# Kernel tuning notes

Hardware: AMD Instinct MI355X
Metric: run time of the kernel (lower is better)

Reference implementation:

```python
import jax, jax.numpy as jnp
import numpy as np

SCALE = 256.0  # emulates SharedFxpShift = 8 fixed-point shift


def requant(x):
    # RequantFxpToScaledInt8: shift down by SharedFxpShift and clamp to int8 range
    return jnp.clip(x / SCALE, -128.0, 127.0)


def prelu(x, a):
    return jnp.where(x >= 0, x, a * x)


def _linearize(c):
    # injective encoding of 3D int coords (coords in [-8, 2040) after +8 shift)
    c = c.astype(jnp.int64) + 8
    B = 2048
    return (c[:, 0] * B + c[:, 1]) * B + c[:, 2]


def sparse_conv(coords, feats, W, stride):
    # 3x3x3 submanifold sparse conv: for each kernel offset, hash-lookup the
    # neighbor via sorted linearized coords + searchsorted, gather, matmul.
    # coords [N,3] int32, feats [N,Cin], W [27,Cin,Cout]
    lin = _linearize(coords)
    perm = jnp.argsort(lin)
    slin = lin[perm]
    N = coords.shape[0]
    out = jnp.zeros((N, W.shape[-1]), feats.dtype)
    k = 0
    for dx in (-1, 0, 1):
        for dy in (-1, 0, 1):
            for dz in (-1, 0, 1):
                off = jnp.array([dx, dy, dz], jnp.int32) * stride
                q = _linearize(coords + off[None, :])
                pos = jnp.clip(jnp.searchsorted(slin, q), 0, N - 1)
                hit = slin[pos] == q
                nb = perm[pos]
                f = jnp.where(hit[:, None], feats[nb], 0.0)
                out = out + f @ W[k]
                k += 1
    return out


def setup_inputs() -> dict:
    N, M, C = 200000, 400000, 64
    rng = np.random.default_rng(0)
    # unique parent coords: multiples of 2 in 512^3 grid
    lin = rng.choice(2 ** 24, size=N, replace=False).astype(np.int64)
    px = (lin // (256 * 256)) % 256
    py = (lin // 256) % 256
    pz = lin % 256
    rec_C = (np.stack([px, py, pz], 1) * 2).astype(np.int32)  # [N,3], stride 2
    # exactly M occupied children out of N*8, sorted (row-major mask order)
    child_idx = np.sort(rng.choice(N * 8, size=M, replace=False)).astype(np.int32)
    parent = child_idx // 8
    bit = child_idx % 8
    off = np.stack([(bit >> 2) & 1, (bit >> 1) & 1, bit & 1], 1).astype(np.int32)
    child_C = rec_C[parent] + off  # [M,3], stride 1, unique
    bins1_bits = np.zeros((N, 8), np.int32)
    bins1_bits[parent, bit] = 1
    bins0_bits = rng.integers(0, 2, size=(M, 8)).astype(np.int32)

    key = jax.random.key(0)
    ks = jax.random.split(key, 20)

    def w(k, shape, fan_in):
        return jax.random.normal(k, shape, jnp.float32) / np.sqrt(fan_in)

    inp = {
        "rec_F": jax.random.normal(ks[0], (N, C), jnp.float32) * SCALE,
        "dec_W": w(ks[1], (C + 8, C), C + 8),
        "dec_b": w(ks[2], (C,), 1) * 0.1,
        "dec_a": jnp.full((C,), 0.25, jnp.float32),
        "res_W1": w(ks[3], (27, C, C), 27 * C),
        "res_b1": w(ks[4], (C,), 1) * 0.1,
        "res_a1": jnp.full((C,), 0.25, jnp.float32),
        "res_W2": w(ks[5], (27, C, C), 27 * C),
        "res_b2": w(ks[6], (C,), 1) * 0.1,
        "p0_Wc": w(ks[7], (27, C, C), 27 * C),
        "p0_bc": w(ks[8], (C,), 1) * 0.1,
        "p0_ac": jnp.full((C,), 0.25, jnp.float32),
        "p0_Wl": w(ks[9], (C, C * 8), C),
        "p1_Wc": w(ks[10], (27, C, C), 27 * C),
        "p1_bc": w(ks[11], (C,), 1) * 0.1,
        "p1_ac": jnp.full((C,), 0.25, jnp.float32),
        "p1_Wl": w(ks[12], (C, 255), C),
        "rec_C": jnp.asarray(rec_C),
        "bins1_bits": jnp.asarray(bins1_bits),
        "child_idx": jnp.asarray(child_idx),
        "child_C": jnp.asarray(child_C),
        "bins0_bits": jnp.asarray(bins0_bits),
    }
    return inp


def reference(rec_F, dec_W, dec_b, dec_a, res_W1, res_b1, res_a1, res_W2, res_b2,
              p0_Wc, p0_bc, p0_ac, p0_Wl, p1_Wc, p1_bc, p1_ac, p1_Wl,
              rec_C, bins1_bits, child_idx, child_C, bins0_bits):
    C = dec_W.shape[1]
    # embed (empty Sequential for pred_steps=2): bins1.F << SharedFxpShift
    embed_f = bins1_bits.astype(jnp.float32) * SCALE  # [N,8]
    x = jnp.concatenate([rec_F, embed_f], 1)  # [N, C+8]
    # dec: Requant -> LinearPReLU(C+8 -> C, out32) -> ResBlock(C)
    h = requant(x)
    h = prelu(h @ dec_W + dec_b, dec_a)  # [N,C]
    r = requant(h)
    r = prelu(sparse_conv(rec_C, r, res_W1, 2) + res_b1, res_a1)
    r = requant(r)
    r = sparse_conv(rec_C, r, res_W2, 2) + res_b2
    rec_out = h + r  # [N,C]
    # pred[0]: Requant -> SparseConvPReLU(out8) -> Linear(C -> 8C, out32)
    p = requant(rec_out)
    p = requant(prelu(sparse_conv(rec_C, p, p0_Wc, 2) + p0_bc, p0_ac))
    p = p @ p0_Wl  # [N, 8C]
    # boolean-mask gather of occupied children: reshape [N,8,C] then mask ->
    # equals flat row gather with precomputed sorted child indices
    p = p.reshape(-1, C)[child_idx]  # [M,C]
    # pred[1] (last): Requant -> SparseConvPReLU(out8) -> Linear(C -> 255, out32)
    p = requant(p)
    p = requant(prelu(sparse_conv(child_C, p, p1_Wc, 1) + p1_bc, p1_ac))
    pred_out = p @ p1_Wl  # [M,255]
    # cur_oct = (cur_bins[0].F << bin2oct_kernel).sum(1) - 1
    k = jnp.arange(8, dtype=jnp.int32)
    cur_oct = ((bins0_bits << k).sum(1) - 1).astype(jnp.int16)  # [M]
    return rec_out, pred_out, cur_oct
```

## Files before the change

### kernel.cpp

```cpp
#include <hip/hip_runtime.h>
#include <stdint.h>


typedef short bf16x8 __attribute__((ext_vector_type(8)));
typedef float f32x4 __attribute__((ext_vector_type(4)));

#define EMPTY_KEY 0xFFFFFFFFu

__device__ __forceinline__ float rq(float x) {
  x *= (1.0f / 256.0f);
  return fminf(fmaxf(x, -128.0f), 127.0f);
}

__device__ __forceinline__ short f2b(float f) {
  union { float f; uint32_t u; } v; v.f = f;
  uint32_t u = v.u;
  uint32_t r = (u + 0x7FFFu + ((u >> 16) & 1u)) >> 16;
  return (short)r;
}

__device__ __forceinline__ uint32_t hkey(int x, int y, int z) {
  return ((uint32_t)(x + 8) << 20) | ((uint32_t)(y + 8) << 10) | (uint32_t)(z + 8);
}
__device__ __forceinline__ uint32_t hfun(uint32_t key, uint32_t mask) {
  return (key * 2654435761u) & mask;
}


__global__ void k_fill_u32(uint32_t* p, int n, uint32_t v) {
  int i = blockIdx.x * 256 + threadIdx.x;
  if (i < n) p[i] = v;
}

__global__ void k_hash_insert(const int* __restrict__ coords, int n,
                              uint32_t* __restrict__ keys, int* __restrict__ vals,
                              uint32_t mask) {
  int i = blockIdx.x * 256 + threadIdx.x;
  if (i >= n) return;
  uint32_t key = hkey(coords[i * 3], coords[i * 3 + 1], coords[i * 3 + 2]);
  uint32_t s = hfun(key, mask);
  while (true) {
    uint32_t old = atomicCAS(&keys[s], EMPTY_KEY, key);
    if (old == EMPTY_KEY) { vals[s] = i; return; }
    s = (s + 1) & mask;
  }
}

__global__ void k_build_nbr(const int* __restrict__ coords, int n, int stride,
                            const uint32_t* __restrict__ keys,
                            const int* __restrict__ vals, uint32_t mask,
                            int* __restrict__ nbr) {
  int t = blockIdx.x * 256 + threadIdx.x;
  if (t >= n * 27) return;
  int i = t / 27, k = t % 27;
  int dx = k / 9 - 1, dy = (k / 3) % 3 - 1, dz = k % 3 - 1;
  int x = coords[i * 3] + dx * stride;
  int y = coords[i * 3 + 1] + dy * stride;
  int z = coords[i * 3 + 2] + dz * stride;
  uint32_t key = hkey(x, y, z);
  uint32_t s = hfun(key, mask);
  int res = -1;
  while (true) {
    uint32_t kk = keys[s];
    if (kk == key) { res = vals[s]; break; }
    if (kk == EMPTY_KEY) break;
    s = (s + 1) & mask;
  }
  nbr[(size_t)i * 28 + k] = res;
}

__global__ void k_pack_bits(const int* __restrict__ bins1, int N,
                            int* __restrict__ bitsPacked) {
  int p = blockIdx.x * 256 + threadIdx.x;
  if (p >= N) return;
  int b = 0;
#pragma unroll
  for (int e = 0; e < 8; e++) b |= (bins1[(size_t)p * 8 + e] & 1) << e;
  bitsPacked[p] = b;
}

__global__ void k_parent_start(const int* __restrict__ child_idx, int M,
                               int* __restrict__ ps) {
  int m = blockIdx.x * 256 + threadIdx.x;
  if (m >= M) return;
  int p = child_idx[m] >> 3;
  if (m == 0 || (child_idx[m - 1] >> 3) != p) ps[p] = m;
}

__global__ void k_build_nbr_child(const int* __restrict__ child_C,
                                  const int* __restrict__ child_idx, int M,
                                  const uint32_t* __restrict__ rkeys,
                                  const int* __restrict__ rvals, uint32_t rmask,
                                  const int* __restrict__ bitsPacked,
                                  const int* __restrict__ parentStart,
                                  int* __restrict__ nbr) {
  int t = blockIdx.x * 256 + threadIdx.x;
  if (t >= M * 27) return;
  int m = t / 27, k = t % 27;
  int dx = k / 9 - 1, dy = (k / 3) % 3 - 1, dz = k % 3 - 1;
  int cx = child_C[(size_t)m * 3], cy = child_C[(size_t)m * 3 + 1],
      cz = child_C[(size_t)m * 3 + 2];
  int tx = cx + dx, ty = cy + dy, tz = cz + dz;
  int qx = tx >> 1, qy = ty >> 1, qz = tz >> 1;
  int r;
  if (qx == (cx >> 1) && qy == (cy >> 1) && qz == (cz >> 1)) {
    r = child_idx[m] >> 3;
  } else {
    uint32_t key = hkey(qx * 2, qy * 2, qz * 2);
    uint32_t s = hfun(key, rmask);
    r = -1;
    while (true) {
      uint32_t kk = rkeys[s];
      if (kk == key) { r = rvals[s]; break; }
      if (kk == EMPTY_KEY) break;
      s = (s + 1) & rmask;
    }
  }
  int res = -1;
  if (r >= 0) {
    int bits = bitsPacked[r];
    int bit = ((tx & 1) << 2) | ((ty & 1) << 1) | (tz & 1);
    if ((bits >> bit) & 1)
      res = parentStart[r] + __popc(bits & ((1 << bit) - 1));
  }
  nbr[(size_t)m * 28 + k] = res;
}

__global__ void k_pack_conv(const float* __restrict__ W, short* __restrict__ dst) {
  int gid = blockIdx.x * 256 + threadIdx.x;
  if (gid >= 27 * 2 * 4 * 64) return;
  int lane = gid & 63;
  int c = (gid >> 6) & 3;
  int t = (gid >> 8) & 1;
  int k = gid >> 9;
  int n = c * 16 + (lane & 15);
  int g = lane >> 4;
  bf16x8 v;
#pragma unroll
  for (int e = 0; e < 8; e++) {
    int kk = t * 32 + g * 8 + e;
    v[e] = f2b(W[(k * 64 + kk) * 64 + n]);
  }
  *(bf16x8*)(dst + gid * 8) = v;
}

__global__ void k_pack_dense(const float* __restrict__ W, short* __restrict__ dst,
                             int K, int Ncols, int KT, int CT) {
  int gid = blockIdx.x * 256 + threadIdx.x;
  if (gid >= KT * CT * 64) return;
  int lane = gid & 63;
  int c = (gid >> 6) % CT;
  int t = gid / (64 * CT);
  int n = c * 16 + (lane & 15);
  int g = lane >> 4;
  bf16x8 v;
#pragma unroll
  for (int e = 0; e < 8; e++) {
    int kk = t * 32 + g * 8 + e;
    float val = (kk < K && n < Ncols) ? W[kk * Ncols + n] : 0.0f;
    v[e] = f2b(val);
  }
  *(bf16x8*)(dst + gid * 8) = v;
}

__global__ void __launch_bounds__(256)
k_bucket(const int* __restrict__ child_idx, int M,
         int* __restrict__ lists, int* __restrict__ cnt) {
  __shared__ int lcnt[8];
  __shared__ int lbase[8];
  int tid = threadIdx.x;
  if (tid < 8) lcnt[tid] = 0;
  __syncthreads();
  int m = blockIdx.x * 256 + tid;
  int b = 0, lp = 0;
  if (m < M) {
    b = child_idx[m] & 7;
    lp = atomicAdd(&lcnt[b], 1);
  }
  __syncthreads();
  if (tid < 8) lbase[tid] = atomicAdd(&cnt[tid], lcnt[tid]);
  __syncthreads();
  if (m < M) lists[(size_t)b * M + lbase[b] + lp] = m;
}


__global__ void __launch_bounds__(256)
k_dec(const float* __restrict__ recF, const int* __restrict__ bits,
      const short* __restrict__ wp, const float* __restrict__ bias,
      const float* __restrict__ alpha, float* __restrict__ h32,
      short* __restrict__ hq) {
  int tid = threadIdx.x, wid = tid >> 6, lane = tid & 63;
  int rowbase = blockIdx.x * 64 + wid * 16;
  int lrow = rowbase + (lane & 15);
  int g = lane >> 4;
  f32x4 acc[4] = {};
#pragma unroll
  for (int t = 0; t < 3; t++) {
    bf16x8 a = {0, 0, 0, 0, 0, 0, 0, 0};
    if (t < 2) {
      const float* src = recF + (size_t)lrow * 64 + t * 32 + g * 8;
#pragma unroll
      for (int e = 0; e < 8; e++) a[e] = f2b(rq(src[e]));
    } else if (g == 0) {
      const int* bp = bits + (size_t)lrow * 8;
#pragma unroll
      for (int e = 0; e < 8; e++) a[e] = f2b((float)bp[e]);
    }
#pragma unroll
    for (int c = 0; c < 4; c++) {
      bf16x8 b = *(const bf16x8*)(wp + ((t * 4 + c) * 64 + lane) * 8);
      acc[c] = __builtin_amdgcn_mfma_f32_16x16x32_bf16(a, b, acc[c], 0, 0, 0);
    }
  }
#pragma unroll
  for (int c = 0; c < 4; c++) {
    int col = c * 16 + (lane & 15);
    float bi = bias[col], al = alpha[col];
#pragma unroll
    for (int r = 0; r < 4; r++) {
      int row = rowbase + g * 4 + r;
      float v = acc[c][r] + bi;
      v = v >= 0.0f ? v : al * v;
      h32[(size_t)row * 64 + col] = v;
      hq[(size_t)row * 64 + col] = f2b(rq(v));
    }
  }
}

template <int MODE>
__global__ void __launch_bounds__(256)
k_conv(const short* __restrict__ fin, const int* __restrict__ nbr,
       const short* __restrict__ wp, const float* __restrict__ bias,
       const float* __restrict__ alpha, const float* __restrict__ resid,
       float* __restrict__ out32, short* __restrict__ outq) {
  int tid = threadIdx.x, wid = tid >> 6, lane = tid & 63;
  int rowbase = blockIdx.x * 64 + wid * 16;
  int lrow = rowbase + (lane & 15);
  int g = lane >> 4;

  int4 nv[7];
#pragma unroll
  for (int j = 0; j < 7; j++)
    nv[j] = *(const int4*)(nbr + (size_t)lrow * 28 + j * 4);
  int nbk[28];
#pragma unroll
  for (int j = 0; j < 7; j++) {
    nbk[j * 4 + 0] = nv[j].x;
    nbk[j * 4 + 1] = nv[j].y;
    nbk[j * 4 + 2] = nv[j].z;
    nbk[j * 4 + 3] = nv[j].w;
  }

  f32x4 acc[4] = {};
#pragma unroll
  for (int k = 0; k < 27; k++) {
    if (__any(nbk[k] >= 0)) {
      int nb = nbk[k];
      bf16x8 a0 = {0, 0, 0, 0, 0, 0, 0, 0};
      bf16x8 a1 = {0, 0, 0, 0, 0, 0, 0, 0};
      if (nb >= 0) {
        const short* fp = fin + (size_t)nb * 64 + g * 8;
        a0 = *(const bf16x8*)fp;
        a1 = *(const bf16x8*)(fp + 32);
      }
      const short* wk = wp + k * 4096;
#pragma unroll
      for (int c = 0; c < 4; c++) {
        bf16x8 b0 = *(const bf16x8*)(wk + (c * 64 + lane) * 8);
        acc[c] = __builtin_amdgcn_mfma_f32_16x16x32_bf16(a0, b0, acc[c], 0, 0, 0);
      }
#pragma unroll
      for (int c = 0; c < 4; c++) {
        bf16x8 b1 = *(const bf16x8*)(wk + ((4 + c) * 64 + lane) * 8);
        acc[c] = __builtin_amdgcn_mfma_f32_16x16x32_bf16(a1, b1, acc[c], 0, 0, 0);
      }
    }
  }
#pragma unroll
  for (int c = 0; c < 4; c++) {
    int col = c * 16 + (lane & 15);
    float bi = bias[col];
    float al = (MODE == 0) ? alpha[col] : 0.0f;
#pragma unroll
    for (int r = 0; r < 4; r++) {
      int row = rowbase + g * 4 + r;
      float v = acc[c][r] + bi;
      if (MODE == 0) {
        v = v >= 0.0f ? v : al * v;
        outq[(size_t)row * 64 + col] = f2b(rq(v));
      } else {
        v += resid[(size_t)row * 64 + col];
        out32[(size_t)row * 64 + col] = v;
        outq[(size_t)row * 64 + col] = f2b(rq(v));
      }
    }
  }
}

__global__ void __launch_bounds__(256)
k_p0(const short* __restrict__ qq, const int* __restrict__ child_idx,
     const int* __restrict__ lists, const int* __restrict__ cnt,
     const short* __restrict__ wp, short* __restrict__ tq, int M) {
  int b = blockIdx.y;
  int cb = cnt[b];
  int start = blockIdx.x * 64;
  if (start >= cb) return;
  int tid = threadIdx.x, wid = tid >> 6, lane = tid & 63, g = lane >> 4;
  int posA = start + wid * 16 + (lane & 15);
  int parent = -1;
  if (posA < cb) parent = child_idx[lists[(size_t)b * M + posA]] >> 3;
  f32x4 acc[4] = {};
#pragma unroll
  for (int t = 0; t < 2; t++) {
    bf16x8 a = {0, 0, 0, 0, 0, 0, 0, 0};
    if (parent >= 0) a = *(const bf16x8*)(qq + (size_t)parent * 64 + t * 32 + g * 8);
#pragma unroll
    for (int c = 0; c < 4; c++) {
      bf16x8 bb = *(const bf16x8*)(wp + (((size_t)t * 32 + b * 4 + c) * 64 + lane) * 8);
      acc[c] = __builtin_amdgcn_mfma_f32_16x16x32_bf16(a, bb, acc[c], 0, 0, 0);
    }
  }
#pragma unroll
  for (int r = 0; r < 4; r++) {
    int posD = start + wid * 16 + g * 4 + r;
    if (posD < cb) {
      int m = lists[(size_t)b * M + posD];
#pragma unroll
      for (int c = 0; c < 4; c++) {
        int col = c * 16 + (lane & 15);
        tq[(size_t)m * 64 + col] = f2b(rq(acc[c][r]));
      }
    }
  }
}

__global__ void __launch_bounds__(256)
k_convp1(const short* __restrict__ fin, const int* __restrict__ nbr,
         const short* __restrict__ wp, const float* __restrict__ bias,
         const float* __restrict__ alpha,
         const int* __restrict__ lists, const int* __restrict__ cnt,
         const short* __restrict__ p1wp, float* __restrict__ out, int M) {
  __shared__ short lds[4][16][64];
  __shared__ int mrow[4][16];
  int tid = threadIdx.x, wid = tid >> 6, lane = tid & 63;
  int l15 = lane & 15, g = lane >> 4;

  int pos = blockIdx.x * 64 + wid * 16 + l15;
  int m = -1;
  if (pos < M) {
    int rem = pos, b = 0;
#pragma unroll
    for (int i = 0; i < 7; i++) {
      int ci = cnt[i];
      if (b == i && rem >= ci) { rem -= ci; b = i + 1; }
    }
    m = lists[(size_t)b * M + rem];
  }
  if (g == 0) mrow[wid][l15] = m;

  int4 nv[7];
#pragma unroll
  for (int j = 0; j < 7; j++) {
    if (m >= 0) nv[j] = *(const int4*)(nbr + (size_t)m * 28 + j * 4);
    else nv[j] = make_int4(-1, -1, -1, -1);
  }
  int nbk[28];
#pragma unroll
  for (int j = 0; j < 7; j++) {
    nbk[j * 4 + 0] = nv[j].x;
    nbk[j * 4 + 1] = nv[j].y;
    nbk[j * 4 + 2] = nv[j].z;
    nbk[j * 4 + 3] = nv[j].w;
  }

  f32x4 acc[4] = {};
#pragma unroll
  for (int k = 0; k < 27; k++) {
    if (__any(nbk[k] >= 0)) {
      int nb = nbk[k];
      bf16x8 a0 = {0, 0, 0, 0, 0, 0, 0, 0};
      bf16x8 a1 = {0, 0, 0, 0, 0, 0, 0, 0};
      if (nb >= 0) {
        const short* fp = fin + (size_t)nb * 64 + g * 8;
        a0 = *(const bf16x8*)fp;
        a1 = *(const bf16x8*)(fp + 32);
      }
      const short* wk = wp + k * 4096;
#pragma unroll
      for (int c = 0; c < 4; c++) {
        bf16x8 b0 = *(const bf16x8*)(wk + (c * 64 + lane) * 8);
        acc[c] = __builtin_amdgcn_mfma_f32_16x16x32_bf16(a0, b0, acc[c], 0, 0, 0);
      }
#pragma unroll
      for (int c = 0; c < 4; c++) {
        bf16x8 b1 = *(const bf16x8*)(wk + ((4 + c) * 64 + lane) * 8);
        acc[c] = __builtin_amdgcn_mfma_f32_16x16x32_bf16(a1, b1, acc[c], 0, 0, 0);
      }
    }
  }

#pragma unroll
  for (int c = 0; c < 4; c++) {
    int col = c * 16 + l15;
    float bi = bias[col], al = alpha[col];
#pragma unroll
    for (int r = 0; r < 4; r++) {
      int rowW = g * 4 + r;
      float v = acc[c][r] + bi;
      v = v >= 0.0f ? v : al * v;
      lds[wid][rowW][col ^ ((rowW & 7) << 3)] = f2b(rq(v));
    }
  }
  __syncthreads();

  f32x4 acc2[16] = {};
#pragma unroll
  for (int t = 0; t < 2; t++) {
    bf16x8 a = *(const bf16x8*)&lds[wid][l15][(t * 32 + g * 8) ^ ((l15 & 7) << 3)];
#pragma unroll
    for (int c = 0; c < 16; c++) {
      bf16x8 bb = *(const bf16x8*)(p1wp + ((t * 16 + c) * 64 + lane) * 8);
      acc2[c] = __builtin_amdgcn_mfma_f32_16x16x32_bf16(a, bb, acc2[c], 0, 0, 0);
    }
  }
#pragma unroll
  for (int r = 0; r < 4; r++) {
    int mo = mrow[wid][g * 4 + r];
    if (mo >= 0) {
#pragma unroll
      for (int c = 0; c < 16; c++) {
        int col = c * 16 + l15;
        if (col < 255) out[(size_t)mo * 255 + col] = acc2[c][r];
      }
    }
  }
}

__global__ void k_oct(const int* __restrict__ bins0, float* __restrict__ out, int M) {
  int m = blockIdx.x * 256 + threadIdx.x;
  if (m >= M) return;
  int s = 0;
#pragma unroll
  for (int e = 0; e < 8; e++) s += bins0[(size_t)m * 8 + e] << e;
  out[m] = (float)(s - 1);
}


extern "C" void kernel_launch(void* const* d_in, const int* in_sizes, int n_in,
                              void* d_out, int out_size, void* d_ws, size_t ws_size,
                              hipStream_t stream) {
  const float* rec_F  = (const float*)d_in[0];
  const float* dec_W  = (const float*)d_in[1];
  const float* dec_b  = (const float*)d_in[2];
  const float* dec_a  = (const float*)d_in[3];
  const float* res_W1 = (const float*)d_in[4];
  const float* res_b1 = (const float*)d_in[5];
  const float* res_a1 = (const float*)d_in[6];
  const float* res_W2 = (const float*)d_in[7];
  const float* res_b2 = (const float*)d_in[8];
  const float* p0_Wc  = (const float*)d_in[9];
  const float* p0_bc  = (const float*)d_in[10];
  const float* p0_ac  = (const float*)d_in[11];
  const float* p0_Wl  = (const float*)d_in[12];
  const float* p1_Wc  = (const float*)d_in[13];
  const float* p1_bc  = (const float*)d_in[14];
  const float* p1_ac  = (const float*)d_in[15];
  const float* p1_Wl  = (const float*)d_in[16];
  const int* rec_C    = (const int*)d_in[17];
  const int* bins1    = (const int*)d_in[18];
  const int* child_idx= (const int*)d_in[19];
  const int* child_C  = (const int*)d_in[20];
  const int* bins0    = (const int*)d_in[21];

  const int N = in_sizes[0] / 64;
  const int M = in_sizes[19];

  char* ws = (char*)d_ws;
  size_t off = 0;
  auto alloc = [&](size_t bytes) -> char* {
    char* p = ws + off;
    off += (bytes + 255) & ~(size_t)255;
    return p;
  };
  const int HRB = 19;
  const uint32_t HR = 1u << HRB;
  uint32_t* rkeys = (uint32_t*)alloc((size_t)HR * 4);
  int*      rvals = (int*)alloc((size_t)HR * 4);
  int* nbrR = (int*)alloc((size_t)N * 28 * 4);
  int* nbrC = (int*)alloc((size_t)M * 28 * 4);
  short* wpack = (short*)alloc((size_t)4 * 110592 * 2);
  short* decwp = (short*)alloc((size_t)3 * 4 * 64 * 8 * 2);
  short* p0wp  = (short*)alloc((size_t)2 * 32 * 64 * 8 * 2);
  short* p1wp  = (short*)alloc((size_t)2 * 16 * 64 * 8 * 2);
  short* bufA = (short*)alloc((size_t)N * 64 * 2);
  short* bufB = (short*)alloc((size_t)N * 64 * 2);
  float* h32  = (float*)alloc((size_t)N * 64 * 4);
  short* tq   = (short*)alloc((size_t)M * 64 * 2);
  int* lists  = (int*)alloc((size_t)8 * M * 4);
  int* bcnt   = (int*)alloc(256);
  int* bitsPk = (int*)alloc((size_t)N * 4);
  int* pStart = (int*)alloc((size_t)N * 4);

  float* outRec  = (float*)d_out;
  float* outPred = outRec + (size_t)N * 64;
  float* outOct  = outPred + (size_t)M * 255;

  dim3 B(256);

  k_fill_u32<<<(HR + 255) / 256, B, 0, stream>>>(rkeys, HR, EMPTY_KEY);
  k_fill_u32<<<1, B, 0, stream>>>((uint32_t*)bcnt, 8, 0u);
  k_hash_insert<<<(N + 255) / 256, B, 0, stream>>>(rec_C, N, rkeys, rvals, HR - 1);
  k_pack_bits<<<(N + 255) / 256, B, 0, stream>>>(bins1, N, bitsPk);
  k_parent_start<<<(M + 255) / 256, B, 0, stream>>>(child_idx, M, pStart);
  k_build_nbr<<<(N * 27 + 255) / 256, B, 0, stream>>>(rec_C, N, 2, rkeys, rvals, HR - 1, nbrR);
  k_build_nbr_child<<<(M * 27 + 255) / 256, B, 0, stream>>>(
      child_C, child_idx, M, rkeys, rvals, HR - 1, bitsPk, pStart, nbrC);
  k_pack_conv<<<54, B, 0, stream>>>(res_W1, wpack);
  k_pack_conv<<<54, B, 0, stream>>>(res_W2, wpack + 110592);
  k_pack_conv<<<54, B, 0, stream>>>(p0_Wc, wpack + 221184);
  k_pack_conv<<<54, B, 0, stream>>>(p1_Wc, wpack + 331776);
  k_pack_dense<<<3, B, 0, stream>>>(dec_W, decwp, 72, 64, 3, 4);
  k_pack_dense<<<16, B, 0, stream>>>(p0_Wl, p0wp, 64, 512, 2, 32);
  k_pack_dense<<<8, B, 0, stream>>>(p1_Wl, p1wp, 64, 255, 2, 16);
  k_bucket<<<(M + 255) / 256, B, 0, stream>>>(child_idx, M, lists, bcnt);

  k_dec<<<N / 64, B, 0, stream>>>(rec_F, bins1, decwp, dec_b, dec_a, h32, bufA);
  k_conv<0><<<N / 64, B, 0, stream>>>(bufA, nbrR, wpack, res_b1, res_a1,
                                      nullptr, nullptr, bufB);
  k_conv<1><<<N / 64, B, 0, stream>>>(bufB, nbrR, wpack + 110592, res_b2, nullptr,
                                      h32, outRec, bufA);
  k_conv<0><<<N / 64, B, 0, stream>>>(bufA, nbrR, wpack + 221184, p0_bc, p0_ac,
                                      nullptr, nullptr, bufB);
  k_p0<<<dim3(M / 64, 8), B, 0, stream>>>(bufB, child_idx, lists, bcnt, p0wp, tq, M);
  k_convp1<<<(M + 63) / 64, B, 0, stream>>>(tq, nbrC, wpack + 331776, p1_bc, p1_ac,
                                            lists, bcnt, p1wp, outPred, M);
  k_oct<<<(M + 255) / 256, B, 0, stream>>>(bins0, outOct, M);
}
```

Before: 742.2 us.

## Merge setup kernels into three launches and chunk convp1 dense epilogue

```diff
diff --git a/kernel.cpp b/kernel.cpp
--- a/kernel.cpp
+++ b/kernel.cpp
@@ -27,74 +27,176 @@
 }
 
 
-__global__ void k_fill_u32(uint32_t* p, int n, uint32_t v) {
-  int i = blockIdx.x * 256 + threadIdx.x;
-  if (i < n) p[i] = v;
-}
-
-__global__ void k_hash_insert(const int* __restrict__ coords, int n,
-                              uint32_t* __restrict__ keys, int* __restrict__ vals,
-                              uint32_t mask) {
-  int i = blockIdx.x * 256 + threadIdx.x;
-  if (i >= n) return;
-  uint32_t key = hkey(coords[i * 3], coords[i * 3 + 1], coords[i * 3 + 2]);
-  uint32_t s = hfun(key, mask);
-  while (true) {
-    uint32_t old = atomicCAS(&keys[s], EMPTY_KEY, key);
-    if (old == EMPTY_KEY) { vals[s] = i; return; }
-    s = (s + 1) & mask;
-  }
-}
-
-__global__ void k_build_nbr(const int* __restrict__ coords, int n, int stride,
-                            const uint32_t* __restrict__ keys,
-                            const int* __restrict__ vals, uint32_t mask,
-                            int* __restrict__ nbr) {
-  int t = blockIdx.x * 256 + threadIdx.x;
-  if (t >= n * 27) return;
-  int i = t / 27, k = t % 27;
-  int dx = k / 9 - 1, dy = (k / 3) % 3 - 1, dz = k % 3 - 1;
-  int x = coords[i * 3] + dx * stride;
-  int y = coords[i * 3 + 1] + dy * stride;
-  int z = coords[i * 3 + 2] + dz * stride;
-  uint32_t key = hkey(x, y, z);
-  uint32_t s = hfun(key, mask);
-  int res = -1;
-  while (true) {
-    uint32_t kk = keys[s];
-    if (kk == key) { res = vals[s]; break; }
-    if (kk == EMPTY_KEY) break;
-    s = (s + 1) & mask;
-  }
-  nbr[(size_t)i * 28 + k] = res;
-}
-
-__global__ void k_pack_bits(const int* __restrict__ bins1, int N,
-                            int* __restrict__ bitsPacked) {
-  int p = blockIdx.x * 256 + threadIdx.x;
-  if (p >= N) return;
-  int b = 0;
-#pragma unroll
-  for (int e = 0; e < 8; e++) b |= (bins1[(size_t)p * 8 + e] & 1) << e;
-  bitsPacked[p] = b;
-}
-
-__global__ void k_parent_start(const int* __restrict__ child_idx, int M,
-                               int* __restrict__ ps) {
-  int m = blockIdx.x * 256 + threadIdx.x;
-  if (m >= M) return;
-  int p = child_idx[m] >> 3;
-  if (m == 0 || (child_idx[m - 1] >> 3) != p) ps[p] = m;
-}
-
-__global__ void k_build_nbr_child(const int* __restrict__ child_C,
-                                  const int* __restrict__ child_idx, int M,
-                                  const uint32_t* __restrict__ rkeys,
-                                  const int* __restrict__ rvals, uint32_t rmask,
-                                  const int* __restrict__ bitsPacked,
-                                  const int* __restrict__ parentStart,
-                                  int* __restrict__ nbr) {
-  int t = blockIdx.x * 256 + threadIdx.x;
+__device__ __forceinline__ void pack_conv_elem(const float* __restrict__ W,
+                                               short* __restrict__ dst, int gid) {
+  int lane = gid & 63;
+  int c = (gid >> 6) & 3;
+  int t = (gid >> 8) & 1;
+  int k = gid >> 9;
+  int n = c * 16 + (lane & 15);
+  int g = lane >> 4;
+  bf16x8 v;
+#pragma unroll
+  for (int e = 0; e < 8; e++) {
+    int kk = t * 32 + g * 8 + e;
+    v[e] = f2b(W[(k * 64 + kk) * 64 + n]);
+  }
+  *(bf16x8*)(dst + gid * 8) = v;
+}
+
+__device__ __forceinline__ void pack_dense_elem(const float* __restrict__ W,
+                                                short* __restrict__ dst, int K,
+                                                int Ncols, int KT, int CT, int gid) {
+  if (gid >= KT * CT * 64) return;
+  int lane = gid & 63;
+  int c = (gid >> 6) % CT;
+  int t = gid / (64 * CT);
+  int n = c * 16 + (lane & 15);
+  int g = lane >> 4;
+  bf16x8 v;
+#pragma unroll
+  for (int e = 0; e < 8; e++) {
+    int kk = t * 32 + g * 8 + e;
+    float val = (kk < K && n < Ncols) ? W[kk * Ncols + n] : 0.0f;
+    v[e] = f2b(val);
+  }
+  *(bf16x8*)(dst + gid * 8) = v;
+}
+
+struct SetupA {
+  const float *dec_W, *p0_Wl, *p1_Wl, *res_W1, *res_W2, *p0_Wc, *p1_Wc;
+  const int *bins1, *child_idx, *bins0;
+  uint32_t* rkeys;
+  short *wpack, *decwp, *p0wp, *p1wp;
+  int *bitsPk, *pStart, *bcnt;
+  float* outOct;
+  int N, M;
+};
+
+__global__ void __launch_bounds__(256) k_setupA(SetupA s) {
+  int bid = blockIdx.x, tid = threadIdx.x;
+  if (bid < 2048) {
+    s.rkeys[bid * 256 + tid] = EMPTY_KEY;
+    return;
+  }
+  bid -= 2048;
+  if (bid < 216) {
+    int which = bid / 54, sb = bid % 54;
+    int gid = sb * 256 + tid;
+    if (gid < 27 * 2 * 4 * 64) {
+      const float* W = which == 0 ? s.res_W1 : which == 1 ? s.res_W2
+                     : which == 2 ? s.p0_Wc : s.p1_Wc;
+      pack_conv_elem(W, s.wpack + which * 110592, gid);
+    }
+    return;
+  }
+  bid -= 216;
+  if (bid < 27) {
+    if (bid < 3) pack_dense_elem(s.dec_W, s.decwp, 72, 64, 3, 4, bid * 256 + tid);
+    else if (bid < 19) pack_dense_elem(s.p0_Wl, s.p0wp, 64, 512, 2, 32, (bid - 3) * 256 + tid);
+    else pack_dense_elem(s.p1_Wl, s.p1wp, 64, 255, 2, 16, (bid - 19) * 256 + tid);
+    return;
+  }
+  bid -= 27;
+  int nbN = (s.N + 255) / 256, nbM = (s.M + 255) / 256;
+  if (bid < nbN) {
+    int p = bid * 256 + tid;
+    if (p < s.N) {
+      int b = 0;
+#pragma unroll
+      for (int e = 0; e < 8; e++) b |= (s.bins1[(size_t)p * 8 + e] & 1) << e;
+      s.bitsPk[p] = b;
+    }
+    return;
+  }
+  bid -= nbN;
+  if (bid < nbM) {
+    int m = bid * 256 + tid;
+    if (m < s.M) {
+      int p = s.child_idx[m] >> 3;
+      if (m == 0 || (s.child_idx[m - 1] >> 3) != p) s.pStart[p] = m;
+    }
+    return;
+  }
+  bid -= nbM;
+  if (bid < nbM) {
+    int m = bid * 256 + tid;
+    if (m < s.M) {
+      int ss = 0;
+#pragma unroll
+      for (int e = 0; e < 8; e++) ss += s.bins0[(size_t)m * 8 + e] << e;
+      s.outOct[m] = (float)(ss - 1);
+    }
+    return;
+  }
+  if (tid < 8) s.bcnt[tid] = 0;
+}
+
+__global__ void __launch_bounds__(256)
+k_setupB(const int* __restrict__ rec_C, const int* __restrict__ child_idx,
+         uint32_t* __restrict__ rkeys, int* __restrict__ rvals,
+         int* __restrict__ lists, int* __restrict__ cnt, int N, int M) {
+  int bid = blockIdx.x, tid = threadIdx.x;
+  int nbN = (N + 255) / 256;
+  if (bid < nbN) {
+    int i = bid * 256 + tid;
+    if (i >= N) return;
+    uint32_t key = hkey(rec_C[i * 3], rec_C[i * 3 + 1], rec_C[i * 3 + 2]);
+    uint32_t s = hfun(key, (1u << 19) - 1);
+    while (true) {
+      uint32_t old = atomicCAS(&rkeys[s], EMPTY_KEY, key);
+      if (old == EMPTY_KEY) { rvals[s] = i; return; }
+      s = (s + 1) & ((1u << 19) - 1);
+    }
+  }
+  bid -= nbN;
+  __shared__ int lcnt[8];
+  __shared__ int lbase[8];
+  if (tid < 8) lcnt[tid] = 0;
+  __syncthreads();
+  int m = bid * 256 + tid;
+  int b = 0, lp = 0;
+  if (m < M) {
+    b = child_idx[m] & 7;
+    lp = atomicAdd(&lcnt[b], 1);
+  }
+  __syncthreads();
+  if (tid < 8) lbase[tid] = atomicAdd(&cnt[tid], lcnt[tid]);
+  __syncthreads();
+  if (m < M) lists[(size_t)b * M + lbase[b] + lp] = m;
+}
+
+__global__ void __launch_bounds__(256)
+k_setupC(const int* __restrict__ rec_C, const int* __restrict__ child_C,
+         const int* __restrict__ child_idx,
+         const uint32_t* __restrict__ rkeys, const int* __restrict__ rvals,
+         const int* __restrict__ bitsPacked, const int* __restrict__ parentStart,
+         int* __restrict__ nbrR, int* __restrict__ nbrC, int N, int M) {
+  const uint32_t rmask = (1u << 19) - 1;
+  int bid = blockIdx.x, tid = threadIdx.x;
+  int nbRec = (N * 27 + 255) / 256;
+  if (bid < nbRec) {
+    int t = bid * 256 + tid;
+    if (t >= N * 27) return;
+    int i = t / 27, k = t % 27;
+    int dx = k / 9 - 1, dy = (k / 3) % 3 - 1, dz = k % 3 - 1;
+    int x = rec_C[i * 3] + dx * 2;
+    int y = rec_C[i * 3 + 1] + dy * 2;
+    int z = rec_C[i * 3 + 2] + dz * 2;
+    uint32_t key = hkey(x, y, z);
+    uint32_t s = hfun(key, rmask);
+    int res = -1;
+    while (true) {
+      uint32_t kk = rkeys[s];
+      if (kk == key) { res = rvals[s]; break; }
+      if (kk == EMPTY_KEY) break;
+      s = (s + 1) & rmask;
+    }
+    nbrR[(size_t)i * 28 + k] = res;
+    return;
+  }
+  bid -= nbRec;
+  int t = bid * 256 + tid;
   if (t >= M * 27) return;
   int m = t / 27, k = t % 27;
   int dx = k / 9 - 1, dy = (k / 3) % 3 - 1, dz = k % 3 - 1;
@@ -123,64 +225,7 @@
     if ((bits >> bit) & 1)
       res = parentStart[r] + __popc(bits & ((1 << bit) - 1));
   }
-  nbr[(size_t)m * 28 + k] = res;
-}
-
-__global__ void k_pack_conv(const float* __restrict__ W, short* __restrict__ dst) {
-  int gid = blockIdx.x * 256 + threadIdx.x;
-  if (gid >= 27 * 2 * 4 * 64) return;
-  int lane = gid & 63;
-  int c = (gid >> 6) & 3;
-  int t = (gid >> 8) & 1;
-  int k = gid >> 9;
-  int n = c * 16 + (lane & 15);
-  int g = lane >> 4;
-  bf16x8 v;
-#pragma unroll
-  for (int e = 0; e < 8; e++) {
-    int kk = t * 32 + g * 8 + e;
-    v[e] = f2b(W[(k * 64 + kk) * 64 + n]);
-  }
-  *(bf16x8*)(dst + gid * 8) = v;
-}
-
-__global__ void k_pack_dense(const float* __restrict__ W, short* __restrict__ dst,
-                             int K, int Ncols, int KT, int CT) {
-  int gid = blockIdx.x * 256 + threadIdx.x;
-  if (gid >= KT * CT * 64) return;
-  int lane = gid & 63;
-  int c = (gid >> 6) % CT;
-  int t = gid / (64 * CT);
-  int n = c * 16 + (lane & 15);
-  int g = lane >> 4;
-  bf16x8 v;
-#pragma unroll
-  for (int e = 0; e < 8; e++) {
-    int kk = t * 32 + g * 8 + e;
-    float val = (kk < K && n < Ncols) ? W[kk * Ncols + n] : 0.0f;
-    v[e] = f2b(val);
-  }
-  *(bf16x8*)(dst + gid * 8) = v;
-}
-
-__global__ void __launch_bounds__(256)
-k_bucket(const int* __restrict__ child_idx, int M,
-         int* __restrict__ lists, int* __restrict__ cnt) {
-  __shared__ int lcnt[8];
-  __shared__ int lbase[8];
-  int tid = threadIdx.x;
-  if (tid < 8) lcnt[tid] = 0;
-  __syncthreads();
-  int m = blockIdx.x * 256 + tid;
-  int b = 0, lp = 0;
-  if (m < M) {
-    b = child_idx[m] & 7;
-    lp = atomicAdd(&lcnt[b], 1);
-  }
-  __syncthreads();
-  if (tid < 8) lbase[tid] = atomicAdd(&cnt[tid], lcnt[tid]);
-  __syncthreads();
-  if (m < M) lists[(size_t)b * M + lbase[b] + lp] = m;
+  nbrC[(size_t)m * 28 + k] = res;
 }
 
 
@@ -334,7 +379,7 @@
   }
 }
 
-__global__ void __launch_bounds__(256)
+__global__ void __launch_bounds__(256, 4)
 k_convp1(const short* __restrict__ fin, const int* __restrict__ nbr,
          const short* __restrict__ wp, const float* __restrict__ bias,
          const float* __restrict__ alpha,
@@ -413,36 +458,30 @@
   }
   __syncthreads();
 
-  f32x4 acc2[16] = {};
-#pragma unroll
-  for (int t = 0; t < 2; t++) {
-    bf16x8 a = *(const bf16x8*)&lds[wid][l15][(t * 32 + g * 8) ^ ((l15 & 7) << 3)];
-#pragma unroll
-    for (int c = 0; c < 16; c++) {
-      bf16x8 bb = *(const bf16x8*)(p1wp + ((t * 16 + c) * 64 + lane) * 8);
-      acc2[c] = __builtin_amdgcn_mfma_f32_16x16x32_bf16(a, bb, acc2[c], 0, 0, 0);
-    }
-  }
-#pragma unroll
-  for (int r = 0; r < 4; r++) {
-    int mo = mrow[wid][g * 4 + r];
-    if (mo >= 0) {
-#pragma unroll
-      for (int c = 0; c < 16; c++) {
-        int col = c * 16 + l15;
-        if (col < 255) out[(size_t)mo * 255 + col] = acc2[c][r];
-      }
-    }
-  }
-}
-
-__global__ void k_oct(const int* __restrict__ bins0, float* __restrict__ out, int M) {
-  int m = blockIdx.x * 256 + threadIdx.x;
-  if (m >= M) return;
-  int s = 0;
-#pragma unroll
-  for (int e = 0; e < 8; e++) s += bins0[(size_t)m * 8 + e] << e;
-  out[m] = (float)(s - 1);
+  bf16x8 a0 = *(const bf16x8*)&lds[wid][l15][(g * 8) ^ ((l15 & 7) << 3)];
+  bf16x8 a1 = *(const bf16x8*)&lds[wid][l15][(32 + g * 8) ^ ((l15 & 7) << 3)];
+#pragma unroll
+  for (int grp = 0; grp < 4; grp++) {
+    f32x4 a2[4] = {};
+#pragma unroll
+    for (int c = 0; c < 4; c++) {
+      bf16x8 b0 = *(const bf16x8*)(p1wp + ((grp * 4 + c) * 64 + lane) * 8);
+      a2[c] = __builtin_amdgcn_mfma_f32_16x16x32_bf16(a0, b0, a2[c], 0, 0, 0);
+      bf16x8 b1 = *(const bf16x8*)(p1wp + ((16 + grp * 4 + c) * 64 + lane) * 8);
+      a2[c] = __builtin_amdgcn_mfma_f32_16x16x32_bf16(a1, b1, a2[c], 0, 0, 0);
+    }
+#pragma unroll
+    for (int r = 0; r < 4; r++) {
+      int mo = mrow[wid][g * 4 + r];
+      if (mo >= 0) {
+#pragma unroll
+        for (int c = 0; c < 4; c++) {
+          int col = (grp * 4 + c) * 16 + l15;
+          if (col < 255) out[(size_t)mo * 255 + col] = a2[c][r];
+        }
+      }
+    }
+  }
 }
 
 
@@ -482,8 +521,7 @@
     off += (bytes + 255) & ~(size_t)255;
     return p;
   };
-  const int HRB = 19;
-  const uint32_t HR = 1u << HRB;
+  const uint32_t HR = 1u << 19;
   uint32_t* rkeys = (uint32_t*)alloc((size_t)HR * 4);
   int*      rvals = (int*)alloc((size_t)HR * 4);
   int* nbrR = (int*)alloc((size_t)N * 28 * 4);
@@ -506,23 +544,18 @@
   float* outOct  = outPred + (size_t)M * 255;
 
   dim3 B(256);
-
-  k_fill_u32<<<(HR + 255) / 256, B, 0, stream>>>(rkeys, HR, EMPTY_KEY);
-  k_fill_u32<<<1, B, 0, stream>>>((uint32_t*)bcnt, 8, 0u);
-  k_hash_insert<<<(N + 255) / 256, B, 0, stream>>>(rec_C, N, rkeys, rvals, HR - 1);
-  k_pack_bits<<<(N + 255) / 256, B, 0, stream>>>(bins1, N, bitsPk);
-  k_parent_start<<<(M + 255) / 256, B, 0, stream>>>(child_idx, M, pStart);
-  k_build_nbr<<<(N * 27 + 255) / 256, B, 0, stream>>>(rec_C, N, 2, rkeys, rvals, HR - 1, nbrR);
-  k_build_nbr_child<<<(M * 27 + 255) / 256, B, 0, stream>>>(
-      child_C, child_idx, M, rkeys, rvals, HR - 1, bitsPk, pStart, nbrC);
-  k_pack_conv<<<54, B, 0, stream>>>(res_W1, wpack);
-  k_pack_conv<<<54, B, 0, stream>>>(res_W2, wpack + 110592);
-  k_pack_conv<<<54, B, 0, stream>>>(p0_Wc, wpack + 221184);
-  k_pack_conv<<<54, B, 0, stream>>>(p1_Wc, wpack + 331776);
-  k_pack_dense<<<3, B, 0, stream>>>(dec_W, decwp, 72, 64, 3, 4);
-  k_pack_dense<<<16, B, 0, stream>>>(p0_Wl, p0wp, 64, 512, 2, 32);
-  k_pack_dense<<<8, B, 0, stream>>>(p1_Wl, p1wp, 64, 255, 2, 16);
-  k_bucket<<<(M + 255) / 256, B, 0, stream>>>(child_idx, M, lists, bcnt);
+  int nbN = (N + 255) / 256, nbM = (M + 255) / 256;
+
+  SetupA sa = {dec_W, p0_Wl, p1_Wl, res_W1, res_W2, p0_Wc, p1_Wc,
+               bins1, child_idx, bins0, rkeys, wpack, decwp, p0wp, p1wp,
+               bitsPk, pStart, bcnt, outOct, N, M};
+  int gridA = 2048 + 216 + 27 + nbN + nbM + nbM + 1;
+  k_setupA<<<gridA, B, 0, stream>>>(sa);
+  k_setupB<<<nbN + nbM, B, 0, stream>>>(rec_C, child_idx, rkeys, rvals,
+                                        lists, bcnt, N, M);
+  int gridC = (N * 27 + 255) / 256 + (M * 27 + 255) / 256;
+  k_setupC<<<gridC, B, 0, stream>>>(rec_C, child_C, child_idx, rkeys, rvals,
+                                    bitsPk, pStart, nbrR, nbrC, N, M);
 
   k_dec<<<N / 64, B, 0, stream>>>(rec_F, bins1, decwp, dec_b, dec_a, h32, bufA);
   k_conv<0><<<N / 64, B, 0, stream>>>(bufA, nbrR, wpack, res_b1, res_a1,
@@ -534,5 +567,4 @@
   k_p0<<<dim3(M / 64, 8), B, 0, stream>>>(bufB, child_idx, lists, bcnt, p0wp, tq, M);
   k_convp1<<<(M + 63) / 64, B, 0, stream>>>(tq, nbrC, wpack + 331776, p1_bc, p1_ac,
                                             lists, bcnt, p1wp, outPred, M);
-  k_oct<<<(M + 255) / 256, B, 0, stream>>>(bins0, outOct, M);
-}
+}
```

Result: faster. 690.0 us (-7.0%).
